# Performance work log

Hardware: AMD Instinct MI355X
Metric: run time of the kernel (lower is better)

## Reference

```python
import jax, jax.numpy as jnp
import numpy as np

N = 250_000   # nodes per graph batch
E = 4_000_000 # edges
G = 1024      # graphs (segments)
F_IN, C, D = 6, 64, 5
EPS = 1e-5    # PyG LayerNorm eps


def setup_inputs() -> dict:
    key = jax.random.key(0)
    ks = jax.random.split(key, 30)
    rn = lambda k, s: jax.random.normal(k, s, jnp.float32)
    p = lambda k, s: rn(k, s) * 0.05
    return {
        "x1": rn(ks[0], (N, F_IN)),
        "edge_index1": jax.random.randint(ks[1], (2, E), 0, N, jnp.int32),
        "batch1": jnp.sort(jax.random.randint(ks[2], (N,), 0, G, jnp.int32)),
        "x2": rn(ks[3], (N, F_IN)),
        "edge_index2": jax.random.randint(ks[4], (2, E), 0, N, jnp.int32),
        "batch2": jnp.sort(jax.random.randint(ks[5], (N,), 0, G, jnp.int32)),
        "d1": rn(ks[6], (G, D)),
        "d2": rn(ks[7], (G, D)),
        # GIN MLP 1: Linear(6,64) -> ReLU -> Linear(64,64)
        "W1": p(ks[8], (F_IN, C)), "b1": jnp.zeros((C,), jnp.float32),
        "W2": p(ks[9], (C, C)),    "b2": jnp.zeros((C,), jnp.float32),
        "ln1w": jnp.ones((C,), jnp.float32), "ln1b": jnp.zeros((C,), jnp.float32),
        # GIN MLP 2
        "W3": p(ks[10], (C, C)), "b3": jnp.zeros((C,), jnp.float32),
        "W4": p(ks[11], (C, C)), "b4": jnp.zeros((C,), jnp.float32),
        "ln2w": jnp.ones((C,), jnp.float32), "ln2b": jnp.zeros((C,), jnp.float32),
        # head: Linear(138,128) -> Linear(128,64) -> Linear(64,1)
        "Wf1": p(ks[12], (2 * C + 2 * D, 128)), "bf1": jnp.zeros((128,), jnp.float32),
        "Wf2": p(ks[13], (128, 64)),            "bf2": jnp.zeros((64,), jnp.float32),
        "Wo": p(ks[14], (64, 1)),               "bo": jnp.zeros((1,), jnp.float32),
    }


def _gin(x, src, dst, Wa, ba, Wb, bb):
    # GINConv, eps=0: h = x + sum_{j in N(i)} x_j ; then MLP (dropout = eval identity)
    agg = jax.ops.segment_sum(x[src], dst, num_segments=N)
    h = x + agg
    h = jax.nn.relu(h @ Wa + ba)
    return h @ Wb + bb


def _graph_layernorm(x, batch, w, b):
    # PyG LayerNorm mode='graph': normalize over all nodes AND channels per graph
    cnt = jax.ops.segment_sum(jnp.ones((x.shape[0],), x.dtype), batch, num_segments=G)
    norm = jnp.maximum(cnt, 1.0) * x.shape[-1]          # [G]
    mean = jax.ops.segment_sum(x.sum(-1), batch, num_segments=G) / norm
    xc = x - mean[batch][:, None]
    var = jax.ops.segment_sum((xc * xc).sum(-1), batch, num_segments=G) / norm
    out = xc * jax.lax.rsqrt(var + EPS)[batch][:, None]
    return out * w + b


def _forward_one(x, edge_index, batch, W1, b1, W2, b2, ln1w, ln1b, W3, b3, W4, b4, ln2w, ln2b):
    src, dst = edge_index[0], edge_index[1]
    x = jax.nn.relu(_graph_layernorm(_gin(x, src, dst, W1, b1, W2, b2), batch, ln1w, ln1b))
    x = jax.nn.relu(_graph_layernorm(_gin(x, src, dst, W3, b3, W4, b4), batch, ln2w, ln2b))
    add = jax.ops.segment_sum(x, batch, num_segments=G)  # [G, C]
    cnt = jax.ops.segment_sum(jnp.ones((x.shape[0],), x.dtype), batch, num_segments=G)
    mean = add / jnp.maximum(cnt, 1.0)[:, None]
    return add + mean


def reference(x1, edge_index1, batch1, x2, edge_index2, batch2, d1, d2,
              W1, b1, W2, b2, ln1w, ln1b, W3, b3, W4, b4, ln2w, ln2b,
              Wf1, bf1, Wf2, bf2, Wo, bo):
    shared = (W1, b1, W2, b2, ln1w, ln1b, W3, b3, W4, b4, ln2w, ln2b)
    emb1 = _forward_one(x1, edge_index1, batch1, *shared)
    emb2 = _forward_one(x2, edge_index2, batch2, *shared)
    h = jnp.concatenate([emb1, emb2, d1, d2], axis=1)    # [G, 138]
    h = jax.nn.relu(h @ Wf1 + bf1)                       # dropout identity (eval)
    h = jax.nn.relu(h @ Wf2 + bf2)
    return h @ Wo + bo                                   # [G, 1]
```

## Files before the change

### kernel.cpp

```cpp
#include <hip/hip_runtime.h>

typedef unsigned short ushort_t;
typedef __attribute__((ext_vector_type(8))) short bf16x8;
typedef __attribute__((ext_vector_type(4))) float f32x4;

#define FIN 6
#define CAP 20480
#define LNCAP 384

__device__ __forceinline__ float blo(unsigned u) { return __uint_as_float(u << 16); }
__device__ __forceinline__ float bhi(unsigned u) { return __uint_as_float(u & 0xffff0000u); }
__device__ __forceinline__ ushort_t f2b(float f) {
  unsigned u = __float_as_uint(f);
  unsigned r = (u + 0x7fffu + ((u >> 16) & 1u)) >> 16;
  return (ushort_t)r;
}
__device__ __forceinline__ float b2f(ushort_t s) { return __uint_as_float(((unsigned)s) << 16); }
__device__ __forceinline__ unsigned pk2(float lo, float hi) {
  return ((unsigned)f2b(hi) << 16) | (unsigned)f2b(lo);
}
union U4F { uint4 u; bf16x8 v; };
__device__ __forceinline__ bf16x8 asfrag(uint4 u) { U4F x; x.u = u; return x.v; }

#define EPT 32
#define TILE 8192

__global__ void k_binit(int* __restrict__ ecur, int* __restrict__ off, int nbuk, int N, int E) {
  int t = threadIdx.x;
  if (t < nbuk) ecur[t] = t * CAP;
  if (t == 0) off[N] = E;
}

__global__ __launch_bounds__(256) void k_bscatter(const int* __restrict__ src,
    const int* __restrict__ dst, int* __restrict__ ecur,
    unsigned* __restrict__ ebuf, int E, int nbuk) {
  __shared__ int cnt[256];
  __shared__ int gbase[256];
  int t = threadIdx.x;
  cnt[t] = 0;
  __syncthreads();
  int base = blockIdx.x * TILE;
  unsigned pk[EPT];
  unsigned pv[EPT];
  #pragma unroll
  for (int k = 0; k < EPT; ++k) {
    int e = base + k * 256 + t;
    if (e < E) {
      int d = dst[e];
      int b = d >> 10;
      int r = atomicAdd(&cnt[b], 1);
      pk[k] = (unsigned)b | ((unsigned)r << 8);
      pv[k] = ((unsigned)(d & 1023) << 18) | (unsigned)src[e];
    } else {
      pk[k] = 0xFFFFFFFFu;
    }
  }
  __syncthreads();
  if (t < nbuk && cnt[t] > 0) gbase[t] = atomicAdd(&ecur[t], cnt[t]);
  __syncthreads();
  #pragma unroll
  for (int k = 0; k < EPT; ++k) {
    if (pk[k] != 0xFFFFFFFFu) {
      int b = pk[k] & 255;
      int r = pk[k] >> 8;
      ebuf[gbase[b] + r] = pv[k];
    }
  }
}

__global__ __launch_bounds__(256) void k_bscan2(const int* __restrict__ ecur,
    int* __restrict__ ebase, int nbuk) {
  __shared__ int lds[256];
  int t = threadIdx.x;
  int s = (t < nbuk) ? (ecur[t] - t * CAP) : 0;
  lds[t] = s; __syncthreads();
  int acc = s;
  for (int o = 1; o < 256; o <<= 1) {
    int add = (t >= o) ? lds[t - o] : 0;
    __syncthreads();
    acc += add; lds[t] = acc;
    __syncthreads();
  }
  if (t < nbuk) ebase[t] = acc - s;
}

__global__ __launch_bounds__(256) void k_bcsr(const unsigned* __restrict__ ebuf,
    const int* __restrict__ ecur, const int* __restrict__ ebase,
    int* __restrict__ off, int* __restrict__ csr, int N) {
  __shared__ int hist[1024];
  __shared__ int lofs[1024];
  __shared__ int sc[256];
  int b = blockIdx.x, t = threadIdx.x;
  int nb0 = b << 10;
  int bn = N - nb0; if (bn > 1024) bn = 1024;
  int s_beg = b * CAP, s_end = ecur[b];
  int base = ebase[b];
  #pragma unroll
  for (int k = 0; k < 4; ++k) hist[t * 4 + k] = 0;
  __syncthreads();
  for (int e = s_beg + t; e < s_end; e += 256) atomicAdd(&hist[ebuf[e] >> 18], 1);
  __syncthreads();
  int h0 = hist[t * 4 + 0], h1 = hist[t * 4 + 1], h2 = hist[t * 4 + 2], h3 = hist[t * 4 + 3];
  int s = h0 + h1 + h2 + h3;
  sc[t] = s; __syncthreads();
  int acc = s;
  for (int o = 1; o < 256; o <<= 1) {
    int add = (t >= o) ? sc[t - o] : 0;
    __syncthreads();
    acc += add; sc[t] = acc;
    __syncthreads();
  }
  int run = acc - s;
  lofs[t * 4 + 0] = run; run += h0;
  lofs[t * 4 + 1] = run; run += h1;
  lofs[t * 4 + 2] = run; run += h2;
  lofs[t * 4 + 3] = run;
  __syncthreads();
  #pragma unroll
  for (int k = 0; k < 4; ++k) {
    int j = t * 4 + k;
    if (j < bn) off[nb0 + j] = base + lofs[j];
  }
  __syncthreads();
  for (int e = s_beg + t; e < s_end; e += 256) {
    unsigned p = ebuf[e];
    int r = atomicAdd(&lofs[p >> 18], 1);
    csr[base + r] = (int)(p & 0x3FFFFu);
  }
}

__global__ void k_prep(const float* __restrict__ x, const int* __restrict__ batch,
                       unsigned* __restrict__ xb, int* __restrict__ gstart, int n, int G) {
  int tt = blockIdx.x * 256 + threadIdx.x;
  if (tt < n * 4) {
    int i = tt >> 2, k = tt & 3;
    unsigned v = 0;
    if (k < 3) {
      float2 f = *(const float2*)(x + (size_t)i * 6 + k * 2);
      v = pk2(f.x, f.y);
    }
    xb[tt] = v;
  }
  if (tt < n) {
    int b = batch[tt];
    if (tt == 0) { for (int g = 0; g <= b; ++g) gstart[g] = 0; }
    else { int pb = batch[tt - 1]; for (int g = pb + 1; g <= b; ++g) gstart[g] = tt; }
    if (tt == n - 1) { for (int g = b + 1; g <= G; ++g) gstart[g] = n; }
  }
}

__global__ void k_wpack(const float* __restrict__ W2, const float* __restrict__ W3,
                        const float* __restrict__ W4, uint4* __restrict__ wfrag) {
  int idx = blockIdx.x * 256 + threadIdx.x;
  if (idx >= 3 * 512) return;
  int widx = idx >> 9, rem = idx & 511;
  int mt = rem >> 7, kh = (rem >> 6) & 1, l = rem & 63;
  int g = l >> 4, c = l & 15;
  const float* W = (widx == 0) ? W2 : (widx == 1) ? W3 : W4;
  int k0 = kh * 32 + g * 8;
  int col = mt * 16 + c;
  uint4 v;
  v.x = pk2(W[(k0 + 0) * 64 + col], W[(k0 + 1) * 64 + col]);
  v.y = pk2(W[(k0 + 2) * 64 + col], W[(k0 + 3) * 64 + col]);
  v.z = pk2(W[(k0 + 4) * 64 + col], W[(k0 + 5) * 64 + col]);
  v.w = pk2(W[(k0 + 6) * 64 + col], W[(k0 + 7) * 64 + col]);
  wfrag[idx] = v;
}

#define ACC6(u) { a0 += blo(u.x); a1 += bhi(u.x); a2 += blo(u.y); a3 += bhi(u.y); a4 += blo(u.z); a5 += bhi(u.z); }
__global__ __launch_bounds__(256) void k_gin1f(const uint4* __restrict__ xb4,
    const int* __restrict__ off, const int* __restrict__ csr,
    const float* __restrict__ W1, const float* __restrict__ b1,
    const uint4* __restrict__ wf2, const float* __restrict__ b2,
    ushort_t* __restrict__ hr, int n) {
  __shared__ __align__(16) ushort_t t1s[32][72];
  __shared__ float sh[4][8][FIN];
  int t = threadIdx.x, w = t >> 6, lane = t & 63;
  int nd = lane >> 3, sl = lane & 7;
  int nb0 = blockIdx.x * 32;
  int i = nb0 + w * 8 + nd;

  float w1r[FIN];
  #pragma unroll
  for (int k = 0; k < FIN; ++k) w1r[k] = W1[k * 64 + lane];
  float bb1 = b1[lane];

  float a0 = 0, a1 = 0, a2 = 0, a3 = 0, a4 = 0, a5 = 0;
  if (i < n) {
    int e0 = off[i], e1 = off[i + 1];
    int e = e0 + sl;
    for (; e + 8 < e1; e += 16) {
      uint4 u = xb4[csr[e]];
      uint4 v = xb4[csr[e + 8]];
      ACC6(u); ACC6(v);
    }
    if (e < e1) { uint4 u = xb4[csr[e]]; ACC6(u); }
    if (sl == 0) { uint4 u = xb4[i]; ACC6(u); }
  }
  #pragma unroll
  for (int m = 1; m < 8; m <<= 1) {
    a0 += __shfl_xor(a0, m); a1 += __shfl_xor(a1, m); a2 += __shfl_xor(a2, m);
    a3 += __shfl_xor(a3, m); a4 += __shfl_xor(a4, m); a5 += __shfl_xor(a5, m);
  }
  if (sl < FIN) {
    float v = (sl == 0) ? a0 : (sl == 1) ? a1 : (sl == 2) ? a2 : (sl == 3) ? a3 : (sl == 4) ? a4 : a5;
    sh[w][nd][sl] = v;
  }
  #pragma unroll
  for (int nd2 = 0; nd2 < 8; ++nd2) {
    float h = bb1;
    #pragma unroll
    for (int k = 0; k < FIN; ++k) h = fmaf(sh[w][nd2][k], w1r[k], h);
    t1s[w * 8 + nd2][lane] = f2b(fmaxf(h, 0.f));
  }
  __syncthreads();
  if (w < 2) {
    int g = lane >> 4, c = lane & 15;
    bf16x8 af[4][2];
    #pragma unroll
    for (int mt = 0; mt < 4; ++mt)
      #pragma unroll
      for (int kh = 0; kh < 2; ++kh) af[mt][kh] = asfrag(wf2[(mt * 2 + kh) * 64 + lane]);
    int r0 = w * 16 + c;
    bf16x8 bf0 = asfrag(*(const uint4*)&t1s[r0][8 * g]);
    bf16x8 bf1 = asfrag(*(const uint4*)&t1s[r0][8 * g + 32]);
    f32x4 acc[4];
    #pragma unroll
    for (int mt = 0; mt < 4; ++mt) {
      acc[mt] = (f32x4){b2[mt * 16 + 4 * g + 0], b2[mt * 16 + 4 * g + 1],
                        b2[mt * 16 + 4 * g + 2], b2[mt * 16 + 4 * g + 3]};
      acc[mt] = __builtin_amdgcn_mfma_f32_16x16x32_bf16(af[mt][0], bf0, acc[mt], 0, 0, 0);
      acc[mt] = __builtin_amdgcn_mfma_f32_16x16x32_bf16(af[mt][1], bf1, acc[mt], 0, 0, 0);
    }
    #pragma unroll
    for (int mt = 0; mt < 4; ++mt) {
      uint2 pv;
      pv.x = pk2(acc[mt][0], acc[mt][1]);
      pv.y = pk2(acc[mt][2], acc[mt][3]);
      *(uint2*)&t1s[r0][mt * 16 + 4 * g] = pv;
    }
    int n2 = lane >> 2, ch = (lane & 3) * 16;
    uint4 s0 = *(const uint4*)&t1s[w * 16 + n2][ch];
    uint4 s1 = *(const uint4*)&t1s[w * 16 + n2][ch + 8];
    int orow = nb0 + w * 16 + n2;
    if (orow < n) {
      uint4* op = (uint4*)(hr + (size_t)orow * 64);
      op[(lane & 3) * 2] = s0;
      op[(lane & 3) * 2 + 1] = s1;
    }
  }
}

#define ACC8(u) { a0 += blo(u.x); a1 += bhi(u.x); a2 += blo(u.y); a3 += bhi(u.y); \
                  a4 += blo(u.z); a5 += bhi(u.z); a6 += blo(u.w); a7 += bhi(u.w); }
__global__ __launch_bounds__(256) void k_agg64(const ushort_t* __restrict__ hb,
    const int* __restrict__ off, const int* __restrict__ csr,
    ushort_t* __restrict__ aggb, int n) {
  int t = threadIdx.x, w = t >> 6, lane = t & 63;
  int i = blockIdx.x * 4 + w;
  if (i >= n) return;
  int grp = lane >> 3, sl = lane & 7;
  int e0 = off[i], e1 = off[i + 1];
  const uint4* hb4 = (const uint4*)hb;
  float a0 = 0, a1 = 0, a2 = 0, a3 = 0, a4 = 0, a5 = 0, a6 = 0, a7 = 0;
  int e = e0 + grp;
  for (; e + 8 < e1; e += 16) {
    int sa = csr[e], sb = csr[e + 8];
    uint4 ua = hb4[(size_t)sa * 8 + sl];
    uint4 ub = hb4[(size_t)sb * 8 + sl];
    ACC8(ua); ACC8(ub);
  }
  if (e < e1) {
    int sa = csr[e];
    uint4 ua = hb4[(size_t)sa * 8 + sl];
    ACC8(ua);
  }
  #pragma unroll
  for (int m = 8; m < 64; m <<= 1) {
    a0 += __shfl_xor(a0, m); a1 += __shfl_xor(a1, m); a2 += __shfl_xor(a2, m);
    a3 += __shfl_xor(a3, m); a4 += __shfl_xor(a4, m); a5 += __shfl_xor(a5, m);
    a6 += __shfl_xor(a6, m); a7 += __shfl_xor(a7, m);
  }
  if (grp == 0) {
    uint4 us = hb4[(size_t)i * 8 + sl];
    ACC8(us);
    uint4 o;
    o.x = pk2(a0, a1); o.y = pk2(a2, a3); o.z = pk2(a4, a5); o.w = pk2(a6, a7);
    ((uint4*)aggb)[(size_t)i * 8 + sl] = o;
  }
}

__global__ __launch_bounds__(256) void k_mlp2_mfma(const ushort_t* __restrict__ aggb,
    const uint4* __restrict__ wf3, const float* __restrict__ b3,
    const uint4* __restrict__ wf4, const float* __restrict__ b4,
    ushort_t* __restrict__ zb, int n) {
  __shared__ __align__(16) ushort_t lds[4][16][72];
  int t = threadIdx.x, w = t >> 6, l = t & 63;
  int g = l >> 4, c = l & 15;
  bf16x8 a3[4][2], a4[4][2];
  #pragma unroll
  for (int mt = 0; mt < 4; ++mt)
    #pragma unroll
    for (int kh = 0; kh < 2; ++kh) {
      a3[mt][kh] = asfrag(wf3[(mt * 2 + kh) * 64 + l]);
      a4[mt][kh] = asfrag(wf4[(mt * 2 + kh) * 64 + l]);
    }
  float bs3[4][4], bs4[4][4];
  #pragma unroll
  for (int mt = 0; mt < 4; ++mt)
    #pragma unroll
    for (int r = 0; r < 4; ++r) {
      bs3[mt][r] = b3[mt * 16 + 4 * g + r];
      bs4[mt][r] = b4[mt * 16 + 4 * g + r];
    }
  int ntile = (n + 15) >> 4;
  for (int tau = blockIdx.x * 4 + w; tau < ntile; tau += gridDim.x * 4) {
    int nb = tau << 4;
    int row = nb + c; if (row >= n) row = n - 1;
    const uint4* rp = (const uint4*)(aggb + (size_t)row * 64);
    bf16x8 bf0 = asfrag(rp[g]);
    bf16x8 bf1 = asfrag(rp[g + 4]);
    f32x4 acc[4];
    #pragma unroll
    for (int mt = 0; mt < 4; ++mt) {
      acc[mt] = (f32x4){bs3[mt][0], bs3[mt][1], bs3[mt][2], bs3[mt][3]};
      acc[mt] = __builtin_amdgcn_mfma_f32_16x16x32_bf16(a3[mt][0], bf0, acc[mt], 0, 0, 0);
      acc[mt] = __builtin_amdgcn_mfma_f32_16x16x32_bf16(a3[mt][1], bf1, acc[mt], 0, 0, 0);
    }
    #pragma unroll
    for (int mt = 0; mt < 4; ++mt) {
      uint2 pv;
      pv.x = pk2(fmaxf(acc[mt][0], 0.f), fmaxf(acc[mt][1], 0.f));
      pv.y = pk2(fmaxf(acc[mt][2], 0.f), fmaxf(acc[mt][3], 0.f));
      *(uint2*)&lds[w][c][mt * 16 + 4 * g] = pv;
    }
    bf16x8 h0 = asfrag(*(const uint4*)&lds[w][c][8 * g]);
    bf16x8 h1 = asfrag(*(const uint4*)&lds[w][c][8 * g + 32]);
    f32x4 ac2[4];
    #pragma unroll
    for (int mt = 0; mt < 4; ++mt) {
      ac2[mt] = (f32x4){bs4[mt][0], bs4[mt][1], bs4[mt][2], bs4[mt][3]};
      ac2[mt] = __builtin_amdgcn_mfma_f32_16x16x32_bf16(a4[mt][0], h0, ac2[mt], 0, 0, 0);
      ac2[mt] = __builtin_amdgcn_mfma_f32_16x16x32_bf16(a4[mt][1], h1, ac2[mt], 0, 0, 0);
    }
    #pragma unroll
    for (int mt = 0; mt < 4; ++mt) {
      uint2 pv;
      pv.x = pk2(ac2[mt][0], ac2[mt][1]);
      pv.y = pk2(ac2[mt][2], ac2[mt][3]);
      *(uint2*)&lds[w][c][mt * 16 + 4 * g] = pv;
    }
    int n2 = l >> 2, ch = (l & 3) * 16;
    uint4 s0 = *(const uint4*)&lds[w][n2][ch];
    uint4 s1 = *(const uint4*)&lds[w][n2][ch + 8];
    int orow = nb + n2;
    if (orow < n) {
      uint4* op = (uint4*)(zb + (size_t)orow * 64);
      op[(l & 3) * 2] = s0;
      op[(l & 3) * 2 + 1] = s1;
    }
  }
}

__global__ __launch_bounds__(256) void k_ln1(const ushort_t* __restrict__ hr,
    const int* __restrict__ gstart, const float* __restrict__ w, const float* __restrict__ bb,
    ushort_t* __restrict__ hb) {
  __shared__ uint4 st[LNCAP * 8];
  __shared__ float l1[256], l2[256];
  __shared__ float mm[2];
  int g = blockIdx.x, t = threadIdx.x;
  int s0 = gstart[g], s1 = gstart[g + 1], cnt = s1 - s0;
  const uint4* src = (const uint4*)hr + (size_t)s0 * 8;
  int nch = cnt * 8;
  bool fit = cnt <= LNCAP;
  float s = 0.f, ss = 0.f;
  for (int j = t; j < nch; j += 256) {
    uint4 u = src[j];
    if (fit) st[j] = u;
    float v0 = blo(u.x), v1 = bhi(u.x), v2 = blo(u.y), v3 = bhi(u.y);
    float v4 = blo(u.z), v5 = bhi(u.z), v6 = blo(u.w), v7 = bhi(u.w);
    s += ((v0 + v1) + (v2 + v3)) + ((v4 + v5) + (v6 + v7));
    ss += ((v0 * v0 + v1 * v1) + (v2 * v2 + v3 * v3)) + ((v4 * v4 + v5 * v5) + (v6 * v6 + v7 * v7));
  }
  l1[t] = s; l2[t] = ss;
  __syncthreads();
  for (int o = 128; o > 0; o >>= 1) {
    if (t < o) { l1[t] += l1[t + o]; l2[t] += l2[t + o]; }
    __syncthreads();
  }
  if (t == 0) {
    float cf = (float)cnt;
    float norm = fmaxf(cf, 1.f) * 64.f;
    float mean = l1[0] / norm;
    float var = fmaxf(l2[0] / norm - mean * mean, 0.f);
    mm[0] = mean; mm[1] = rsqrtf(var + 1e-5f);
  }
  __syncthreads();
  float mean = mm[0], inv = mm[1];
  uint4* dst = (uint4*)hb + (size_t)s0 * 8;
  for (int j = t; j < nch; j += 256) {
    uint4 u = fit ? st[j] : src[j];
    int q = j & 7;
    float4 w0 = *(const float4*)(w + q * 8);
    float4 w1 = *(const float4*)(w + q * 8 + 4);
    float4 c0 = *(const float4*)(bb + q * 8);
    float4 c1 = *(const float4*)(bb + q * 8 + 4);
    uint4 o;
    o.x = pk2(fmaxf((blo(u.x) - mean) * inv * w0.x + c0.x, 0.f),
              fmaxf((bhi(u.x) - mean) * inv * w0.y + c0.y, 0.f));
    o.y = pk2(fmaxf((blo(u.y) - mean) * inv * w0.z + c0.z, 0.f),
              fmaxf((bhi(u.y) - mean) * inv * w0.w + c0.w, 0.f));
    o.z = pk2(fmaxf((blo(u.z) - mean) * inv * w1.x + c1.x, 0.f),
              fmaxf((bhi(u.z) - mean) * inv * w1.y + c1.y, 0.f));
    o.w = pk2(fmaxf((blo(u.w) - mean) * inv * w1.z + c1.z, 0.f),
              fmaxf((bhi(u.w) - mean) * inv * w1.w + c1.w, 0.f));
    dst[j] = o;
  }
}

__global__ __launch_bounds__(256) void k_ln2pool(const ushort_t* __restrict__ zb,
    const int* __restrict__ gstart, const float* __restrict__ w, const float* __restrict__ bb,
    float* __restrict__ emb) {
  __shared__ unsigned st[LNCAP * 32];
  __shared__ float l1[256], l2[256];
  __shared__ float mm[2];
  int g = blockIdx.x, t = threadIdx.x;
  int s0 = gstart[g], s1 = gstart[g + 1], cnt = s1 - s0;
  const unsigned* src = (const unsigned*)zb + (size_t)s0 * 32;
  int nu = cnt * 32;
  bool fit = cnt <= LNCAP;
  float s = 0.f, ss = 0.f;
  for (int j = t; j < nu; j += 256) {
    unsigned u = src[j];
    if (fit) st[j] = u;
    float v0 = blo(u), v1 = bhi(u);
    s += v0 + v1;
    ss += v0 * v0 + v1 * v1;
  }
  l1[t] = s; l2[t] = ss;
  __syncthreads();
  for (int o = 128; o > 0; o >>= 1) {
    if (t < o) { l1[t] += l1[t + o]; l2[t] += l2[t + o]; }
    __syncthreads();
  }
  if (t == 0) {
    float cf = (float)cnt;
    float norm = fmaxf(cf, 1.f) * 64.f;
    float mean = l1[0] / norm;
    float var = fmaxf(l2[0] / norm - mean * mean, 0.f);
    mm[0] = mean; mm[1] = rsqrtf(var + 1e-5f);
  }
  __syncthreads();
  float mean = mm[0], inv = mm[1];
  int c2 = t & 31, sub = t >> 5;
  float w0 = w[c2 * 2], w1 = w[c2 * 2 + 1], b0 = bb[c2 * 2], b1v = bb[c2 * 2 + 1];
  float acc0 = 0.f, acc1 = 0.f;
  for (int i = sub; i < cnt; i += 8) {
    unsigned u = fit ? st[i * 32 + c2] : src[(size_t)i * 32 + c2];
    acc0 += fmaxf((blo(u) - mean) * inv * w0 + b0, 0.f);
    acc1 += fmaxf((bhi(u) - mean) * inv * w1 + b1v, 0.f);
  }
  __syncthreads();
  l1[t] = acc0; l2[t] = acc1;
  __syncthreads();
  if (sub == 0) {
    float t0 = 0.f, t1v = 0.f;
    #pragma unroll
    for (int sx = 0; sx < 8; ++sx) { t0 += l1[sx * 32 + c2]; t1v += l2[sx * 32 + c2]; }
    float cf = fmaxf((float)cnt, 1.f);
    emb[g * 64 + c2 * 2]     = t0 + t0 / cf;
    emb[g * 64 + c2 * 2 + 1] = t1v + t1v / cf;
  }
}

__global__ __launch_bounds__(128) void k_head(const float* __restrict__ emb1,
    const float* __restrict__ emb2, const float* __restrict__ d1, const float* __restrict__ d2,
    const float* __restrict__ Wf1, const float* __restrict__ bf1,
    const float* __restrict__ Wf2, const float* __restrict__ bf2,
    const float* __restrict__ Wo, const float* __restrict__ bo, float* __restrict__ out) {
  int g = blockIdx.x, t = threadIdx.x;
  __shared__ float v[138], h1s[128], h2s[64];
  if (t < 64) v[t] = emb1[g * 64 + t];
  else v[t] = emb2[g * 64 + (t - 64)];
  if (t < 5) v[128 + t] = d1[g * 5 + t];
  else if (t < 10) v[133 + (t - 5)] = d2[g * 5 + (t - 5)];
  __syncthreads();
  float a = bf1[t];
  for (int k = 0; k < 138; ++k) a = fmaf(v[k], Wf1[k * 128 + t], a);
  h1s[t] = fmaxf(a, 0.f);
  __syncthreads();
  if (t < 64) {
    float a2 = bf2[t];
    #pragma unroll 8
    for (int k = 0; k < 128; ++k) a2 = fmaf(h1s[k], Wf2[k * 64 + t], a2);
    h2s[t] = fmaxf(a2, 0.f);
  }
  __syncthreads();
  if (t == 0) {
    float s = bo[0];
    for (int k = 0; k < 64; ++k) s += h2s[k] * Wo[k];
    out[g] = s;
  }
}

extern "C" void kernel_launch(void* const* d_in, const int* in_sizes, int n_in,
                              void* d_out, int out_size, void* d_ws, size_t ws_size,
                              hipStream_t stream) {
  const float* x1     = (const float*)d_in[0];
  const int*   ei1    = (const int*)d_in[1];
  const int*   batch1 = (const int*)d_in[2];
  const float* x2     = (const float*)d_in[3];
  const int*   ei2    = (const int*)d_in[4];
  const int*   batch2 = (const int*)d_in[5];
  const float* d1     = (const float*)d_in[6];
  const float* d2     = (const float*)d_in[7];
  const float* W1  = (const float*)d_in[8],  *b1  = (const float*)d_in[9];
  const float* W2  = (const float*)d_in[10], *b2  = (const float*)d_in[11];
  const float* ln1w = (const float*)d_in[12], *ln1b = (const float*)d_in[13];
  const float* W3  = (const float*)d_in[14], *b3  = (const float*)d_in[15];
  const float* W4  = (const float*)d_in[16], *b4  = (const float*)d_in[17];
  const float* ln2w = (const float*)d_in[18], *ln2b = (const float*)d_in[19];
  const float* Wf1 = (const float*)d_in[20], *bf1 = (const float*)d_in[21];
  const float* Wf2 = (const float*)d_in[22], *bf2 = (const float*)d_in[23];
  const float* Wo  = (const float*)d_in[24], *bo  = (const float*)d_in[25];
  float* out = (float*)d_out;

  const int N = in_sizes[0] / FIN;
  const int G = in_sizes[6] / 5;
  const int E1 = in_sizes[1] / 2;
  const int E2 = in_sizes[4] / 2;
  const int Emax = (E1 > E2) ? E1 : E2;
  const int NBUK = (N + 1023) >> 10;

  char* p = (char*)d_ws;
  auto alloc = [&](size_t bytes) { void* r = p; p += (bytes + 255) & ~(size_t)255; return r; };
  int*      off    = (int*)alloc((size_t)(N + 1) * 4);
  int*      ecur   = (int*)alloc(256 * 4);
  int*      ebase  = (int*)alloc(257 * 4);
  int*      csr    = (int*)alloc((size_t)Emax * 4);
  int*      gstart = (int*)alloc((size_t)(G + 1) * 4);
  uint4*    wfrag  = (uint4*)alloc(3 * 512 * 16);
  unsigned* xb     = (unsigned*)alloc((size_t)N * 16);
  ushort_t* hr     = (ushort_t*)alloc((size_t)N * 64 * 2);
  ushort_t* hb     = (ushort_t*)alloc((size_t)N * 64 * 2);
  float*    emb1   = (float*)alloc((size_t)G * 64 * 4);
  float*    emb2   = (float*)alloc((size_t)G * 64 * 4);
  ushort_t* aggb = hr;
  ushort_t* zb   = hb;
  unsigned* ebuf = (unsigned*)hb;

  const uint4* wf2 = wfrag;
  const uint4* wf3 = wfrag + 512;
  const uint4* wf4 = wfrag + 1024;

  const int GRID_W  = (N + 3) / 4;
  const int GRID_F  = (N + 31) / 32;
  const int GRID_P  = (N * 4 + 255) / 256;

  k_wpack<<<6, 256, 0, stream>>>(W2, W3, W4, wfrag);

  auto run_graph = [&](const float* x, const int* ei, const int* batch, int E, float* emb) {
    const int* src = ei;
    const int* dst = ei + E;
    const int SCAT = (E + TILE - 1) / TILE;
    k_binit<<<1, 256, 0, stream>>>(ecur, off, NBUK, N, E);
    k_bscatter<<<SCAT, 256, 0, stream>>>(src, dst, ecur, ebuf, E, NBUK);
    k_bscan2<<<1, 256, 0, stream>>>(ecur, ebase, NBUK);
    k_bcsr<<<NBUK, 256, 0, stream>>>(ebuf, ecur, ebase, off, csr, N);
    k_prep<<<GRID_P, 256, 0, stream>>>(x, batch, xb, gstart, N, G);

    k_gin1f<<<GRID_F, 256, 0, stream>>>((const uint4*)xb, off, csr, W1, b1, wf2, b2, hr, N);
    k_ln1<<<G, 256, 0, stream>>>(hr, gstart, ln1w, ln1b, hb);
    k_agg64<<<GRID_W, 256, 0, stream>>>(hb, off, csr, aggb, N);
    k_mlp2_mfma<<<2048, 256, 0, stream>>>(aggb, wf3, b3, wf4, b4, zb, N);
    k_ln2pool<<<G, 256, 0, stream>>>(zb, gstart, ln2w, ln2b, emb);
  };

  run_graph(x1, ei1, batch1, E1, emb1);
  run_graph(x2, ei2, batch2, E2, emb2);
  k_head<<<G, 128, 0, stream>>>(emb1, emb2, d1, d2, Wf1, bf1, Wf2, bf2, Wo, bo, out);
}
```

Baseline: 645.2 us.

## Batch both graphs into one combined node/edge space and run a single pipeline

The two graph passes are merged: node and edge indices of the second graph are offset by N and its graph ids by G, so CSR build, GIN layers, layernorms and pooling each launch once over 2N nodes and 2G graphs. This halves the kernel launch count and gives each kernel twice the parallel work, which should fill the GPU better during the small serial kernels. The edge-packing bit fields are widened to 19 bits for source and 512 buckets, so the scatter kernel uses 512-thread blocks. The first layernorm now writes in place, and the aggregation accumulators are rewritten as float2 pairs, likely to encourage packed adds.

```diff
diff --git a/kernel.cpp b/kernel.cpp
--- a/kernel.cpp
+++ b/kernel.cpp
@@ -15,42 +15,47 @@
   unsigned r = (u + 0x7fffu + ((u >> 16) & 1u)) >> 16;
   return (ushort_t)r;
 }
-__device__ __forceinline__ float b2f(ushort_t s) { return __uint_as_float(((unsigned)s) << 16); }
 __device__ __forceinline__ unsigned pk2(float lo, float hi) {
   return ((unsigned)f2b(hi) << 16) | (unsigned)f2b(lo);
 }
 union U4F { uint4 u; bf16x8 v; };
 __device__ __forceinline__ bf16x8 asfrag(uint4 u) { U4F x; x.u = u; return x.v; }
 
-#define EPT 32
+#define EPT 16
 #define TILE 8192
 
-__global__ void k_binit(int* __restrict__ ecur, int* __restrict__ off, int nbuk, int N, int E) {
+__global__ __launch_bounds__(512) void k_binit(int* __restrict__ ecur, int* __restrict__ off,
+                                               int nbuk, int N2, int Etot) {
   int t = threadIdx.x;
   if (t < nbuk) ecur[t] = t * CAP;
-  if (t == 0) off[N] = E;
-}
-
-__global__ __launch_bounds__(256) void k_bscatter(const int* __restrict__ src,
-    const int* __restrict__ dst, int* __restrict__ ecur,
-    unsigned* __restrict__ ebuf, int E, int nbuk) {
-  __shared__ int cnt[256];
-  __shared__ int gbase[256];
+  if (t == 0) off[N2] = Etot;
+}
+
+__global__ __launch_bounds__(512) void k_bscatter(
+    const int* __restrict__ src1, const int* __restrict__ dst1, int E1,
+    const int* __restrict__ src2, const int* __restrict__ dst2, int E2,
+    int* __restrict__ ecur, unsigned* __restrict__ ebuf, int N, int nbuk) {
+  __shared__ int cnt[512];
+  __shared__ int gbase[512];
   int t = threadIdx.x;
   cnt[t] = 0;
   __syncthreads();
-  int base = blockIdx.x * TILE;
+  int tile = blockIdx.x;
+  int T1 = (E1 + TILE - 1) / TILE;
+  const int* srcp; const int* dstp; int Elim, ofs, base;
+  if (tile < T1) { srcp = src1; dstp = dst1; Elim = E1; ofs = 0; base = tile * TILE; }
+  else { srcp = src2; dstp = dst2; Elim = E2; ofs = N; base = (tile - T1) * TILE; }
   unsigned pk[EPT];
   unsigned pv[EPT];
   #pragma unroll
   for (int k = 0; k < EPT; ++k) {
-    int e = base + k * 256 + t;
-    if (e < E) {
-      int d = dst[e];
+    int e = base + k * 512 + t;
+    if (e < Elim) {
+      int d = dstp[e] + ofs;
       int b = d >> 10;
       int r = atomicAdd(&cnt[b], 1);
-      pk[k] = (unsigned)b | ((unsigned)r << 8);
-      pv[k] = ((unsigned)(d & 1023) << 18) | (unsigned)src[e];
+      pk[k] = (unsigned)b | ((unsigned)r << 9);
+      pv[k] = ((unsigned)(d & 1023) << 19) | (unsigned)(srcp[e] + ofs);
     } else {
       pk[k] = 0xFFFFFFFFu;
     }
@@ -61,21 +66,21 @@
   #pragma unroll
   for (int k = 0; k < EPT; ++k) {
     if (pk[k] != 0xFFFFFFFFu) {
-      int b = pk[k] & 255;
-      int r = pk[k] >> 8;
+      int b = pk[k] & 511;
+      int r = pk[k] >> 9;
       ebuf[gbase[b] + r] = pv[k];
     }
   }
 }
 
-__global__ __launch_bounds__(256) void k_bscan2(const int* __restrict__ ecur,
+__global__ __launch_bounds__(512) void k_bscan2(const int* __restrict__ ecur,
     int* __restrict__ ebase, int nbuk) {
-  __shared__ int lds[256];
+  __shared__ int lds[512];
   int t = threadIdx.x;
   int s = (t < nbuk) ? (ecur[t] - t * CAP) : 0;
   lds[t] = s; __syncthreads();
   int acc = s;
-  for (int o = 1; o < 256; o <<= 1) {
+  for (int o = 1; o < 512; o <<= 1) {
     int add = (t >= o) ? lds[t - o] : 0;
     __syncthreads();
     acc += add; lds[t] = acc;
@@ -86,19 +91,19 @@
 
 __global__ __launch_bounds__(256) void k_bcsr(const unsigned* __restrict__ ebuf,
     const int* __restrict__ ecur, const int* __restrict__ ebase,
-    int* __restrict__ off, int* __restrict__ csr, int N) {
+    int* __restrict__ off, int* __restrict__ csr, int N2) {
   __shared__ int hist[1024];
   __shared__ int lofs[1024];
   __shared__ int sc[256];
   int b = blockIdx.x, t = threadIdx.x;
   int nb0 = b << 10;
-  int bn = N - nb0; if (bn > 1024) bn = 1024;
+  int bn = N2 - nb0; if (bn > 1024) bn = 1024;
   int s_beg = b * CAP, s_end = ecur[b];
   int base = ebase[b];
   #pragma unroll
   for (int k = 0; k < 4; ++k) hist[t * 4 + k] = 0;
   __syncthreads();
-  for (int e = s_beg + t; e < s_end; e += 256) atomicAdd(&hist[ebuf[e] >> 18], 1);
+  for (int e = s_beg + t; e < s_end; e += 256) atomicAdd(&hist[ebuf[e] >> 19], 1);
   __syncthreads();
   int h0 = hist[t * 4 + 0], h1 = hist[t * 4 + 1], h2 = hist[t * 4 + 2], h3 = hist[t * 4 + 3];
   int s = h0 + h1 + h2 + h3;
@@ -124,28 +129,36 @@
   __syncthreads();
   for (int e = s_beg + t; e < s_end; e += 256) {
     unsigned p = ebuf[e];
-    int r = atomicAdd(&lofs[p >> 18], 1);
-    csr[base + r] = (int)(p & 0x3FFFFu);
-  }
-}
-
-__global__ void k_prep(const float* __restrict__ x, const int* __restrict__ batch,
-                       unsigned* __restrict__ xb, int* __restrict__ gstart, int n, int G) {
+    int r = atomicAdd(&lofs[p >> 19], 1);
+    csr[base + r] = (int)(p & 0x7FFFFu);
+  }
+}
+
+__global__ void k_prep(const float* __restrict__ x1, const float* __restrict__ x2,
+                       const int* __restrict__ batch1, const int* __restrict__ batch2,
+                       unsigned* __restrict__ xb, int* __restrict__ gstart,
+                       int N, int G) {
+  int N2 = 2 * N, G2 = 2 * G;
   int tt = blockIdx.x * 256 + threadIdx.x;
-  if (tt < n * 4) {
+  if (tt < N2 * 4) {
     int i = tt >> 2, k = tt & 3;
     unsigned v = 0;
     if (k < 3) {
-      float2 f = *(const float2*)(x + (size_t)i * 6 + k * 2);
+      const float* xp = (i < N) ? (x1 + (size_t)i * 6) : (x2 + (size_t)(i - N) * 6);
+      float2 f = *(const float2*)(xp + k * 2);
       v = pk2(f.x, f.y);
     }
     xb[tt] = v;
   }
-  if (tt < n) {
-    int b = batch[tt];
-    if (tt == 0) { for (int g = 0; g <= b; ++g) gstart[g] = 0; }
-    else { int pb = batch[tt - 1]; for (int g = pb + 1; g <= b; ++g) gstart[g] = tt; }
-    if (tt == n - 1) { for (int g = b + 1; g <= G; ++g) gstart[g] = n; }
+  if (tt < N2) {
+    int i = tt;
+    int b = (i < N) ? batch1[i] : (batch2[i - N] + G);
+    if (i == 0) { for (int g = 0; g <= b; ++g) gstart[g] = 0; }
+    else {
+      int pb = (i - 1 < N) ? batch1[i - 1] : (batch2[i - 1 - N] + G);
+      for (int g = pb + 1; g <= b; ++g) gstart[g] = i;
+    }
+    if (i == N2 - 1) { for (int g = b + 1; g <= G2; ++g) gstart[g] = N2; }
   }
 }
 
@@ -251,8 +264,10 @@
   }
 }
 
-#define ACC8(u) { a0 += blo(u.x); a1 += bhi(u.x); a2 += blo(u.y); a3 += bhi(u.y); \
-                  a4 += blo(u.z); a5 += bhi(u.z); a6 += blo(u.w); a7 += bhi(u.w); }
+__device__ __forceinline__ float2 up2(unsigned v) { return make_float2(blo(v), bhi(v)); }
+#define PACC(u) { float2 q0 = up2(u.x), q1 = up2(u.y), q2 = up2(u.z), q3 = up2(u.w); \
+                  c0.x += q0.x; c0.y += q0.y; c1.x += q1.x; c1.y += q1.y; \
+                  c2.x += q2.x; c2.y += q2.y; c3.x += q3.x; c3.y += q3.y; }
 __global__ __launch_bounds__(256) void k_agg64(const ushort_t* __restrict__ hb,
     const int* __restrict__ off, const int* __restrict__ csr,
     ushort_t* __restrict__ aggb, int n) {
@@ -262,30 +277,32 @@
   int grp = lane >> 3, sl = lane & 7;
   int e0 = off[i], e1 = off[i + 1];
   const uint4* hb4 = (const uint4*)hb;
-  float a0 = 0, a1 = 0, a2 = 0, a3 = 0, a4 = 0, a5 = 0, a6 = 0, a7 = 0;
+  float2 c0 = {0, 0}, c1 = {0, 0}, c2 = {0, 0}, c3 = {0, 0};
   int e = e0 + grp;
   for (; e + 8 < e1; e += 16) {
     int sa = csr[e], sb = csr[e + 8];
     uint4 ua = hb4[(size_t)sa * 8 + sl];
     uint4 ub = hb4[(size_t)sb * 8 + sl];
-    ACC8(ua); ACC8(ub);
+    PACC(ua); PACC(ub);
   }
   if (e < e1) {
     int sa = csr[e];
     uint4 ua = hb4[(size_t)sa * 8 + sl];
-    ACC8(ua);
+    PACC(ua);
   }
   #pragma unroll
   for (int m = 8; m < 64; m <<= 1) {
-    a0 += __shfl_xor(a0, m); a1 += __shfl_xor(a1, m); a2 += __shfl_xor(a2, m);
-    a3 += __shfl_xor(a3, m); a4 += __shfl_xor(a4, m); a5 += __shfl_xor(a5, m);
-    a6 += __shfl_xor(a6, m); a7 += __shfl_xor(a7, m);
+    c0.x += __shfl_xor(c0.x, m); c0.y += __shfl_xor(c0.y, m);
+    c1.x += __shfl_xor(c1.x, m); c1.y += __shfl_xor(c1.y, m);
+    c2.x += __shfl_xor(c2.x, m); c2.y += __shfl_xor(c2.y, m);
+    c3.x += __shfl_xor(c3.x, m); c3.y += __shfl_xor(c3.y, m);
   }
   if (grp == 0) {
     uint4 us = hb4[(size_t)i * 8 + sl];
-    ACC8(us);
+    PACC(us);
     uint4 o;
-    o.x = pk2(a0, a1); o.y = pk2(a2, a3); o.z = pk2(a4, a5); o.w = pk2(a6, a7);
+    o.x = pk2(c0.x, c0.y); o.y = pk2(c1.x, c1.y);
+    o.z = pk2(c2.x, c2.y); o.w = pk2(c3.x, c3.y);
     ((uint4*)aggb)[(size_t)i * 8 + sl] = o;
   }
 }
@@ -362,15 +379,14 @@
   }
 }
 
-__global__ __launch_bounds__(256) void k_ln1(const ushort_t* __restrict__ hr,
-    const int* __restrict__ gstart, const float* __restrict__ w, const float* __restrict__ bb,
-    ushort_t* __restrict__ hb) {
+__global__ __launch_bounds__(256) void k_ln1(ushort_t* __restrict__ hr,
+    const int* __restrict__ gstart, const float* __restrict__ w, const float* __restrict__ bb) {
   __shared__ uint4 st[LNCAP * 8];
   __shared__ float l1[256], l2[256];
   __shared__ float mm[2];
   int g = blockIdx.x, t = threadIdx.x;
   int s0 = gstart[g], s1 = gstart[g + 1], cnt = s1 - s0;
-  const uint4* src = (const uint4*)hr + (size_t)s0 * 8;
+  uint4* src = (uint4*)hr + (size_t)s0 * 8;
   int nch = cnt * 8;
   bool fit = cnt <= LNCAP;
   float s = 0.f, ss = 0.f;
@@ -397,7 +413,6 @@
   }
   __syncthreads();
   float mean = mm[0], inv = mm[1];
-  uint4* dst = (uint4*)hb + (size_t)s0 * 8;
   for (int j = t; j < nch; j += 256) {
     uint4 u = fit ? st[j] : src[j];
     int q = j & 7;
@@ -414,7 +429,7 @@
               fmaxf((bhi(u.z) - mean) * inv * w1.y + c1.y, 0.f));
     o.w = pk2(fmaxf((blo(u.w) - mean) * inv * w1.z + c1.z, 0.f),
               fmaxf((bhi(u.w) - mean) * inv * w1.w + c1.w, 0.f));
-    dst[j] = o;
+    src[j] = o;
   }
 }
 
@@ -529,54 +544,49 @@
   const int G = in_sizes[6] / 5;
   const int E1 = in_sizes[1] / 2;
   const int E2 = in_sizes[4] / 2;
-  const int Emax = (E1 > E2) ? E1 : E2;
-  const int NBUK = (N + 1023) >> 10;
+  const int N2 = 2 * N;
+  const int Etot = E1 + E2;
+  const int NBUK = (N2 + 1023) >> 10;
 
   char* p = (char*)d_ws;
   auto alloc = [&](size_t bytes) { void* r = p; p += (bytes + 255) & ~(size_t)255; return r; };
-  int*      off    = (int*)alloc((size_t)(N + 1) * 4);
-  int*      ecur   = (int*)alloc(256 * 4);
-  int*      ebase  = (int*)alloc(257 * 4);
-  int*      csr    = (int*)alloc((size_t)Emax * 4);
-  int*      gstart = (int*)alloc((size_t)(G + 1) * 4);
+  int*      off    = (int*)alloc((size_t)(N2 + 1) * 4);
+  int*      ecur   = (int*)alloc(512 * 4);
+  int*      ebase  = (int*)alloc(513 * 4);
+  int*      csr    = (int*)alloc((size_t)Etot * 4);
+  int*      gstart = (int*)alloc((size_t)(2 * G + 1) * 4);
   uint4*    wfrag  = (uint4*)alloc(3 * 512 * 16);
-  unsigned* xb     = (unsigned*)alloc((size_t)N * 16);
-  ushort_t* hr     = (ushort_t*)alloc((size_t)N * 64 * 2);
-  ushort_t* hb     = (ushort_t*)alloc((size_t)N * 64 * 2);
-  float*    emb1   = (float*)alloc((size_t)G * 64 * 4);
-  float*    emb2   = (float*)alloc((size_t)G * 64 * 4);
-  ushort_t* aggb = hr;
-  ushort_t* zb   = hb;
-  unsigned* ebuf = (unsigned*)hb;
+  ushort_t* bufA   = (ushort_t*)alloc((size_t)N2 * 64 * 2);
+  ushort_t* bufB   = (ushort_t*)alloc((size_t)N2 * 64 * 2);
+  float*    emb    = (float*)alloc((size_t)2 * G * 64 * 4);
+
+  unsigned* xb   = (unsigned*)bufB;
+  unsigned* ebuf = (unsigned*)((char*)bufB + (size_t)N2 * 16);
+  ushort_t* hr   = bufA;
+  ushort_t* aggb = bufB;
+  ushort_t* zb   = bufA;
 
   const uint4* wf2 = wfrag;
   const uint4* wf3 = wfrag + 512;
   const uint4* wf4 = wfrag + 1024;
 
-  const int GRID_W  = (N + 3) / 4;
-  const int GRID_F  = (N + 31) / 32;
-  const int GRID_P  = (N * 4 + 255) / 256;
+  const int SCAT   = (E1 + TILE - 1) / TILE + (E2 + TILE - 1) / TILE;
+  const int GRID_F = (N2 + 31) / 32;
+  const int GRID_W = (N2 + 3) / 4;
+  const int GRID_P = (N2 * 4 + 255) / 256;
 
   k_wpack<<<6, 256, 0, stream>>>(W2, W3, W4, wfrag);
-
-  auto run_graph = [&](const float* x, const int* ei, const int* batch, int E, float* emb) {
-    const int* src = ei;
-    const int* dst = ei + E;
-    const int SCAT = (E + TILE - 1) / TILE;
-    k_binit<<<1, 256, 0, stream>>>(ecur, off, NBUK, N, E);
-    k_bscatter<<<SCAT, 256, 0, stream>>>(src, dst, ecur, ebuf, E, NBUK);
-    k_bscan2<<<1, 256, 0, stream>>>(ecur, ebase, NBUK);
-    k_bcsr<<<NBUK, 256, 0, stream>>>(ebuf, ecur, ebase, off, csr, N);
-    k_prep<<<GRID_P, 256, 0, stream>>>(x, batch, xb, gstart, N, G);
-
-    k_gin1f<<<GRID_F, 256, 0, stream>>>((const uint4*)xb, off, csr, W1, b1, wf2, b2, hr, N);
-    k_ln1<<<G, 256, 0, stream>>>(hr, gstart, ln1w, ln1b, hb);
-    k_agg64<<<GRID_W, 256, 0, stream>>>(hb, off, csr, aggb, N);
-    k_mlp2_mfma<<<2048, 256, 0, stream>>>(aggb, wf3, b3, wf4, b4, zb, N);
-    k_ln2pool<<<G, 256, 0, stream>>>(zb, gstart, ln2w, ln2b, emb);
-  };
-
-  run_graph(x1, ei1, batch1, E1, emb1);
-  run_graph(x2, ei2, batch2, E2, emb2);
-  k_head<<<G, 128, 0, stream>>>(emb1, emb2, d1, d2, Wf1, bf1, Wf2, bf2, Wo, bo, out);
-}
+  k_binit<<<1, 512, 0, stream>>>(ecur, off, NBUK, N2, Etot);
+  k_bscatter<<<SCAT, 512, 0, stream>>>(ei1, ei1 + E1, E1, ei2, ei2 + E2, E2, ecur, ebuf, N, NBUK);
+  k_bscan2<<<1, 512, 0, stream>>>(ecur, ebase, NBUK);
+  k_bcsr<<<NBUK, 256, 0, stream>>>(ebuf, ecur, ebase, off, csr, N2);
+  k_prep<<<GRID_P, 256, 0, stream>>>(x1, x2, batch1, batch2, xb, gstart, N, G);
+
+  k_gin1f<<<GRID_F, 256, 0, stream>>>((const uint4*)xb, off, csr, W1, b1, wf2, b2, hr, N2);
+  k_ln1<<<2 * G, 256, 0, stream>>>(hr, gstart, ln1w, ln1b);
+  k_agg64<<<GRID_W, 256, 0, stream>>>(hr, off, csr, aggb, N2);
+  k_mlp2_mfma<<<2048, 256, 0, stream>>>(aggb, wf3, b3, wf4, b4, zb, N2);
+  k_ln2pool<<<2 * G, 256, 0, stream>>>(zb, gstart, ln2w, ln2b, emb);
+
+  k_head<<<G, 128, 0, stream>>>(emb, emb + (size_t)G * 64, d1, d2, Wf1, bf1, Wf2, bf2, Wo, bo, out);
+}
```

Result: faster. 555.8 us (-13.9%).
